# Kernel optimization log

Hardware: AMD Instinct MI355X
Metric: run time of the kernel (lower is better)

Reference implementation:

```python
import jax, jax.numpy as jnp
import numpy as np

NS, NV = 64, 16
IN_DIM = NS + 3 * NV + 3 * NV + NV  # 176 = 64x0e + 16x1o + 16x1e + 16x0o
W_SHAPES = {'0e': (NS + NV, NS), '1o': (NS + 2 * NV, NV), '1e': (3 * NV, NV), '0o': (2 * NV, NV)}
W_NUMEL = sum(a * b for a, b in W_SHAPES.values())  # 7936
E = 16384
S2 = float(np.sqrt(2.0))
S3 = float(np.sqrt(3.0))


def setup_inputs() -> dict:
    key = jax.random.key(0)
    k1, k2, k3 = jax.random.split(key, 3)
    in_ = jax.random.normal(k1, (E, IN_DIM), dtype=jnp.float32)
    sh = jax.random.normal(k2, (E, 4), dtype=jnp.float32)
    weight = jax.random.normal(k3, (E, W_NUMEL), dtype=jnp.float32)
    return {"in_": in_, "sh": sh, "weight": weight}


def reference(in_, sh, weight):
    lead = in_.shape[:-1]
    # split input irreps (order: 0e, 1o, 1e, 0o)
    x0e = in_[..., :NS]                                       # [..., NS]
    x1o = in_[..., NS:NS + 3 * NV].reshape(lead + (NV, 3))    # [..., NV, 3]
    x1e = in_[..., NS + 3 * NV:NS + 6 * NV].reshape(lead + (NV, 3))
    x0o = in_[..., NS + 6 * NV:]                              # [..., NV]
    sh0 = sh[..., 0]            # [...]
    sh1 = sh[..., 1:]           # [..., 3]
    sh1b = sh1[..., None, :]    # [..., 1, 3]

    # tensor-product paths
    out0e = jnp.concatenate([
        x0e * sh0[..., None],                      # 0e x 0e -> 0e
        jnp.sum(x1o * sh1b, axis=-1) / S3,         # 1o . 1o -> 0e
    ], axis=-1)                                    # [..., NS+NV]
    out1o = jnp.concatenate([
        x0e[..., :, None] * sh1b,                  # 0e x 1o -> 1o
        x1o * sh0[..., None, None],                # 1o x 0e -> 1o
        jnp.cross(x1e, sh1b) / S2,                 # 1e x 1o -> 1o
    ], axis=-2)                                    # [..., NS+2NV, 3]
    out1e = jnp.concatenate([
        jnp.cross(x1o, sh1b) / S2,                 # 1o x 1o -> 1e
        x1e * sh0[..., None, None],                # 1e x 0e -> 1e
        x0o[..., :, None] * sh1b,                  # 0o x 1o -> 1e
    ], axis=-2)                                    # [..., 3NV, 3]
    out0o = jnp.concatenate([
        jnp.sum(x1e * sh1b, axis=-1) / S3,         # 1e . 1o -> 0o
        x0o * sh0[..., None],                      # 0o x 0e -> 0o
    ], axis=-1)                                    # [..., 2NV]

    # per-edge weights, split and path-normalized by 1/sqrt(fan_in)
    wd, off = {}, 0
    for k, (a, b) in W_SHAPES.items():
        wd[k] = weight[..., off:off + a * b].reshape(lead + (a, b)) / float(np.sqrt(a))
        off += a * b

    y0e = jnp.einsum('...i,...io->...o', out0e, wd['0e'])                     # [..., NS]
    y1o = jnp.einsum('...ic,...io->...oc', out1o, wd['1o']).reshape(lead + (3 * NV,))
    y1e = jnp.einsum('...ic,...io->...oc', out1e, wd['1e']).reshape(lead + (3 * NV,))
    y0o = jnp.einsum('...i,...io->...o', out0o, wd['0o'])                     # [..., NV]

    return jnp.concatenate([y0e, y1o, y1e, y0o], axis=-1)  # [..., 176]
```

## Files before the change

### kernel.cpp

```cpp
#include <hip/hip_runtime.h>
#include <math.h>

#define NS 64
#define NV 16
#define IN_DIM 176
#define W_NUMEL 7936
#define OUT_DIM 176

#define OFF_0E 0
#define OFF_1O 5120
#define OFF_1E 6656
#define OFF_0O 7424

__global__ __launch_bounds__(256)
void ftp_kernel(const float* __restrict__ in_,
                const float* __restrict__ sh,
                const float* __restrict__ weight,
                float* __restrict__ out)
{
    __shared__ float s_in[IN_DIM];
    __shared__ float s_sh4[4];
    __shared__ float s_o0e[80];
    __shared__ float s_o1o[96 * 3];
    __shared__ float s_o1e[48 * 3];
    __shared__ float s_o0o[32];

    const int row = blockIdx.x;
    const int t = threadIdx.x;
    const float* __restrict__ inr  = in_    + (size_t)row * IN_DIM;
    const float* __restrict__ wr   = weight + (size_t)row * W_NUMEL;
    float* __restrict__       outr = out    + (size_t)row * OUT_DIM;

    if (t < IN_DIM) s_in[t] = inr[t];
    if (t >= 176 && t < 180) s_sh4[t - 176] = sh[(size_t)row * 4 + (t - 176)];
    __syncthreads();

    const float sh0 = s_sh4[0];
    const float sh1_0 = s_sh4[1], sh1_1 = s_sh4[2], sh1_2 = s_sh4[3];
    const float sh1[3] = {sh1_0, sh1_1, sh1_2};
    const float inv_s3 = 0.5773502691896258f;
    const float inv_s2 = 0.7071067811865476f;

    for (int j = t; j < 544; j += 256) {
        if (j < 80) {
            int i = j;
            float val;
            if (i < 64) {
                val = s_in[i] * sh0;
            } else {
                int v = i - 64;
                val = (s_in[64 + v*3 + 0] * sh1_0 +
                       s_in[64 + v*3 + 1] * sh1_1 +
                       s_in[64 + v*3 + 2] * sh1_2) * inv_s3;
            }
            s_o0e[i] = val;
        } else if (j < 368) {
            int jj = j - 80;
            int i = jj / 3, c = jj % 3;
            float val;
            if (i < 64) {
                val = s_in[i] * sh1[c];
            } else if (i < 80) {
                int v = i - 64;
                val = s_in[64 + v*3 + c] * sh0;
            } else {
                int v = i - 80;
                int c1 = (c + 1) % 3, c2 = (c + 2) % 3;
                val = (s_in[112 + v*3 + c1] * sh1[c2] -
                       s_in[112 + v*3 + c2] * sh1[c1]) * inv_s2;
            }
            s_o1o[jj] = val;
        } else if (j < 512) {
            int jj = j - 368;
            int i = jj / 3, c = jj % 3;
            float val;
            if (i < 16) {
                int v = i;
                int c1 = (c + 1) % 3, c2 = (c + 2) % 3;
                val = (s_in[64 + v*3 + c1] * sh1[c2] -
                       s_in[64 + v*3 + c2] * sh1[c1]) * inv_s2;
            } else if (i < 32) {
                int v = i - 16;
                val = s_in[112 + v*3 + c] * sh0;
            } else {
                int v = i - 32;
                val = s_in[160 + v] * sh1[c];
            }
            s_o1e[jj] = val;
        } else {
            int i = j - 512;
            float val;
            if (i < 16) {
                val = (s_in[112 + i*3 + 0] * sh1_0 +
                       s_in[112 + i*3 + 1] * sh1_1 +
                       s_in[112 + i*3 + 2] * sh1_2) * inv_s3;
            } else {
                val = s_in[160 + (i - 16)] * sh0;
            }
            s_o0o[i] = val;
        }
    }
    __syncthreads();

    const int wave = t >> 6;
    const int l = t & 63;

    if (wave < 2) {
        const int o4 = (wave << 3) + (l & 7);
        const int g  = l >> 3;
        float ax = 0.f, ay = 0.f, az = 0.f, aw = 0.f;
        #pragma unroll
        for (int k = 0; k < 10; ++k) {
            const int i = g + (k << 3);
            const float4 w4 = *reinterpret_cast<const float4*>(wr + OFF_0E + i*64 + 4*o4);
            const float s = s_o0e[i];
            ax += w4.x * s; ay += w4.y * s; az += w4.z * s; aw += w4.w * s;
        }
        #pragma unroll
        for (int m = 8; m <= 32; m <<= 1) {
            ax += __shfl_xor(ax, m);
            ay += __shfl_xor(ay, m);
            az += __shfl_xor(az, m);
            aw += __shfl_xor(aw, m);
        }
        if (g == 0) {
            const float n = 0.11180339887498949f;
            float4 r; r.x = ax*n; r.y = ay*n; r.z = az*n; r.w = aw*n;
            *reinterpret_cast<float4*>(outr + 4*o4) = r;
        }
    } else if (wave == 2) {
        const int o4 = l & 3;
        const int g  = l >> 2;
        float a0x=0,a0y=0,a0z=0,a0w=0;
        float a1x=0,a1y=0,a1z=0,a1w=0;
        float a2x=0,a2y=0,a2z=0,a2w=0;
        #pragma unroll
        for (int k = 0; k < 6; ++k) {
            const int i = g + (k << 4);
            const float4 w4 = *reinterpret_cast<const float4*>(wr + OFF_1O + i*16 + 4*o4);
            const float s0 = s_o1o[i*3 + 0];
            const float s1 = s_o1o[i*3 + 1];
            const float s2 = s_o1o[i*3 + 2];
            a0x += w4.x*s0; a0y += w4.y*s0; a0z += w4.z*s0; a0w += w4.w*s0;
            a1x += w4.x*s1; a1y += w4.y*s1; a1z += w4.z*s1; a1w += w4.w*s1;
            a2x += w4.x*s2; a2y += w4.y*s2; a2z += w4.z*s2; a2w += w4.w*s2;
        }
        #pragma unroll
        for (int m = 4; m <= 32; m <<= 1) {
            a0x += __shfl_xor(a0x, m); a0y += __shfl_xor(a0y, m);
            a0z += __shfl_xor(a0z, m); a0w += __shfl_xor(a0w, m);
            a1x += __shfl_xor(a1x, m); a1y += __shfl_xor(a1y, m);
            a1z += __shfl_xor(a1z, m); a1w += __shfl_xor(a1w, m);
            a2x += __shfl_xor(a2x, m); a2y += __shfl_xor(a2y, m);
            a2z += __shfl_xor(a2z, m); a2w += __shfl_xor(a2w, m);
        }
        if (g == 0) {
            const float n = 0.10206207261596575f;
            const int ob = 4*o4;
            outr[64 + (ob+0)*3 + 0] = a0x*n; outr[64 + (ob+0)*3 + 1] = a1x*n; outr[64 + (ob+0)*3 + 2] = a2x*n;
            outr[64 + (ob+1)*3 + 0] = a0y*n; outr[64 + (ob+1)*3 + 1] = a1y*n; outr[64 + (ob+1)*3 + 2] = a2y*n;
            outr[64 + (ob+2)*3 + 0] = a0z*n; outr[64 + (ob+2)*3 + 1] = a1z*n; outr[64 + (ob+2)*3 + 2] = a2z*n;
            outr[64 + (ob+3)*3 + 0] = a0w*n; outr[64 + (ob+3)*3 + 1] = a1w*n; outr[64 + (ob+3)*3 + 2] = a2w*n;
        }
    } else {
        {
            const int o4 = l & 3;
            const int g  = l >> 2;
            float a0x=0,a0y=0,a0z=0,a0w=0;
            float a1x=0,a1y=0,a1z=0,a1w=0;
            float a2x=0,a2y=0,a2z=0,a2w=0;
            #pragma unroll
            for (int k = 0; k < 3; ++k) {
                const int i = g + (k << 4);
                const float4 w4 = *reinterpret_cast<const float4*>(wr + OFF_1E + i*16 + 4*o4);
                const float s0 = s_o1e[i*3 + 0];
                const float s1 = s_o1e[i*3 + 1];
                const float s2 = s_o1e[i*3 + 2];
                a0x += w4.x*s0; a0y += w4.y*s0; a0z += w4.z*s0; a0w += w4.w*s0;
                a1x += w4.x*s1; a1y += w4.y*s1; a1z += w4.z*s1; a1w += w4.w*s1;
                a2x += w4.x*s2; a2y += w4.y*s2; a2z += w4.z*s2; a2w += w4.w*s2;
            }
            #pragma unroll
            for (int m = 4; m <= 32; m <<= 1) {
                a0x += __shfl_xor(a0x, m); a0y += __shfl_xor(a0y, m);
                a0z += __shfl_xor(a0z, m); a0w += __shfl_xor(a0w, m);
                a1x += __shfl_xor(a1x, m); a1y += __shfl_xor(a1y, m);
                a1z += __shfl_xor(a1z, m); a1w += __shfl_xor(a1w, m);
                a2x += __shfl_xor(a2x, m); a2y += __shfl_xor(a2y, m);
                a2z += __shfl_xor(a2z, m); a2w += __shfl_xor(a2w, m);
            }
            if (g == 0) {
                const float n = 0.14433756729740643f;
                const int ob = 4*o4;
                outr[112 + (ob+0)*3 + 0] = a0x*n; outr[112 + (ob+0)*3 + 1] = a1x*n; outr[112 + (ob+0)*3 + 2] = a2x*n;
                outr[112 + (ob+1)*3 + 0] = a0y*n; outr[112 + (ob+1)*3 + 1] = a1y*n; outr[112 + (ob+1)*3 + 2] = a2y*n;
                outr[112 + (ob+2)*3 + 0] = a0z*n; outr[112 + (ob+2)*3 + 1] = a1z*n; outr[112 + (ob+2)*3 + 2] = a2z*n;
                outr[112 + (ob+3)*3 + 0] = a0w*n; outr[112 + (ob+3)*3 + 1] = a1w*n; outr[112 + (ob+3)*3 + 2] = a2w*n;
            }
        }
        {
            const int o4 = l & 3;
            const int g  = l >> 2;
            float ax = 0.f, ay = 0.f, az = 0.f, aw = 0.f;
            #pragma unroll
            for (int k = 0; k < 2; ++k) {
                const int i = g + (k << 4);
                const float4 w4 = *reinterpret_cast<const float4*>(wr + OFF_0O + i*16 + 4*o4);
                const float s = s_o0o[i];
                ax += w4.x * s; ay += w4.y * s; az += w4.z * s; aw += w4.w * s;
            }
            #pragma unroll
            for (int m = 4; m <= 32; m <<= 1) {
                ax += __shfl_xor(ax, m);
                ay += __shfl_xor(ay, m);
                az += __shfl_xor(az, m);
                aw += __shfl_xor(aw, m);
            }
            if (g == 0) {
                const float n = 0.17677669529663687f;
                float4 r; r.x = ax*n; r.y = ay*n; r.z = az*n; r.w = aw*n;
                *reinterpret_cast<float4*>(outr + 160 + 4*o4) = r;
            }
        }
    }
}

extern "C" void kernel_launch(void* const* d_in, const int* in_sizes, int n_in,
                              void* d_out, int out_size, void* d_ws, size_t ws_size,
                              hipStream_t stream) {
    const float* in_    = (const float*)d_in[0];
    const float* sh     = (const float*)d_in[1];
    const float* weight = (const float*)d_in[2];
    float* out = (float*)d_out;
    const int E = in_sizes[0] / IN_DIM;

    ftp_kernel<<<E, 256, 0, stream>>>(in_, sh, weight, out);
}
```

Measured before the change: 98.85 us.

## Drop block barriers; per-wave input staging with weight loads issued first

Each wave now loads the row's input itself into a private LDS slice and syncs with a wave barrier instead of two block-wide __syncthreads. All weight float4 loads are issued before staging, so global latency overlaps the input fetch. Each wave computes its own tensor-product coefficients in registers instead of going through a shared intermediate buffer. The 1e and 0o reductions are merged into one shuffle loop. The cost is redundant input loads per wave and higher register pressure.

```diff
diff --git a/kernel.cpp b/kernel.cpp
--- a/kernel.cpp
+++ b/kernel.cpp
@@ -1,8 +1,5 @@
 #include <hip/hip_runtime.h>
-#include <math.h>
-
-#define NS 64
-#define NV 16
+
 #define IN_DIM 176
 #define W_NUMEL 7936
 #define OUT_DIM 176
@@ -18,110 +15,65 @@
                 const float* __restrict__ weight,
                 float* __restrict__ out)
 {
-    __shared__ float s_in[IN_DIM];
-    __shared__ float s_sh4[4];
-    __shared__ float s_o0e[80];
-    __shared__ float s_o1o[96 * 3];
-    __shared__ float s_o1e[48 * 3];
-    __shared__ float s_o0o[32];
+    __shared__ float s_in[4 * 192];
 
     const int row = blockIdx.x;
     const int t = threadIdx.x;
-    const float* __restrict__ inr  = in_    + (size_t)row * IN_DIM;
-    const float* __restrict__ wr   = weight + (size_t)row * W_NUMEL;
-    float* __restrict__       outr = out    + (size_t)row * OUT_DIM;
-
-    if (t < IN_DIM) s_in[t] = inr[t];
-    if (t >= 176 && t < 180) s_sh4[t - 176] = sh[(size_t)row * 4 + (t - 176)];
-    __syncthreads();
-
-    const float sh0 = s_sh4[0];
-    const float sh1_0 = s_sh4[1], sh1_1 = s_sh4[2], sh1_2 = s_sh4[3];
-    const float sh1[3] = {sh1_0, sh1_1, sh1_2};
+    const int wave = t >> 6;
+    const int l = t & 63;
+
+    const float* __restrict__ inr = in_    + (size_t)row * IN_DIM;
+    const float* __restrict__ wr  = weight + (size_t)row * W_NUMEL;
+    float* __restrict__       outr= out    + (size_t)row * OUT_DIM;
+    const float* __restrict__ shr = sh     + (size_t)row * 4;
+
+    float* s_my = &s_in[wave * 192];
+
+    const float a0 = inr[l];
+    const float a1 = inr[64 + l];
+    const float a2 = (l < 48) ? inr[128 + l] : 0.0f;
+
+    const float sh0   = shr[0];
+    const float sh1_0 = shr[1], sh1_1 = shr[2], sh1_2 = shr[3];
+
     const float inv_s3 = 0.5773502691896258f;
     const float inv_s2 = 0.7071067811865476f;
 
-    for (int j = t; j < 544; j += 256) {
-        if (j < 80) {
-            int i = j;
-            float val;
-            if (i < 64) {
-                val = s_in[i] * sh0;
-            } else {
-                int v = i - 64;
-                val = (s_in[64 + v*3 + 0] * sh1_0 +
-                       s_in[64 + v*3 + 1] * sh1_1 +
-                       s_in[64 + v*3 + 2] * sh1_2) * inv_s3;
-            }
-            s_o0e[i] = val;
-        } else if (j < 368) {
-            int jj = j - 80;
-            int i = jj / 3, c = jj % 3;
-            float val;
-            if (i < 64) {
-                val = s_in[i] * sh1[c];
-            } else if (i < 80) {
-                int v = i - 64;
-                val = s_in[64 + v*3 + c] * sh0;
-            } else {
-                int v = i - 80;
-                int c1 = (c + 1) % 3, c2 = (c + 2) % 3;
-                val = (s_in[112 + v*3 + c1] * sh1[c2] -
-                       s_in[112 + v*3 + c2] * sh1[c1]) * inv_s2;
-            }
-            s_o1o[jj] = val;
-        } else if (j < 512) {
-            int jj = j - 368;
-            int i = jj / 3, c = jj % 3;
-            float val;
-            if (i < 16) {
-                int v = i;
-                int c1 = (c + 1) % 3, c2 = (c + 2) % 3;
-                val = (s_in[64 + v*3 + c1] * sh1[c2] -
-                       s_in[64 + v*3 + c2] * sh1[c1]) * inv_s2;
-            } else if (i < 32) {
-                int v = i - 16;
-                val = s_in[112 + v*3 + c] * sh0;
-            } else {
-                int v = i - 32;
-                val = s_in[160 + v] * sh1[c];
-            }
-            s_o1e[jj] = val;
-        } else {
-            int i = j - 512;
-            float val;
-            if (i < 16) {
-                val = (s_in[112 + i*3 + 0] * sh1_0 +
-                       s_in[112 + i*3 + 1] * sh1_1 +
-                       s_in[112 + i*3 + 2] * sh1_2) * inv_s3;
-            } else {
-                val = s_in[160 + (i - 16)] * sh0;
-            }
-            s_o0o[i] = val;
-        }
-    }
-    __syncthreads();
-
-    const int wave = t >> 6;
-    const int l = t & 63;
+#define STAGE_AND_WAIT()                                        \
+    do {                                                        \
+        s_my[l] = a0; s_my[64 + l] = a1;                        \
+        if (l < 48) s_my[128 + l] = a2;                         \
+        __builtin_amdgcn_wave_barrier();                        \
+        asm volatile("s_waitcnt lgkmcnt(0)" ::: "memory");      \
+        __builtin_amdgcn_sched_barrier(0);                      \
+    } while (0)
 
     if (wave < 2) {
         const int o4 = (wave << 3) + (l & 7);
         const int g  = l >> 3;
+        float4 w[10];
+        #pragma unroll
+        for (int k = 0; k < 10; ++k)
+            w[k] = *reinterpret_cast<const float4*>(wr + OFF_0E + (g + (k << 3)) * 64 + 4 * o4);
+
+        STAGE_AND_WAIT();
+
+        float s[10];
+        #pragma unroll
+        for (int k = 0; k < 8; ++k) s[k] = s_my[g + (k << 3)] * sh0;
+        s[8] = (s_my[64 + 3*g] * sh1_0 + s_my[65 + 3*g] * sh1_1 + s_my[66 + 3*g] * sh1_2) * inv_s3;
+        s[9] = (s_my[88 + 3*g] * sh1_0 + s_my[89 + 3*g] * sh1_1 + s_my[90 + 3*g] * sh1_2) * inv_s3;
+
         float ax = 0.f, ay = 0.f, az = 0.f, aw = 0.f;
         #pragma unroll
         for (int k = 0; k < 10; ++k) {
-            const int i = g + (k << 3);
-            const float4 w4 = *reinterpret_cast<const float4*>(wr + OFF_0E + i*64 + 4*o4);
-            const float s = s_o0e[i];
-            ax += w4.x * s; ay += w4.y * s; az += w4.z * s; aw += w4.w * s;
+            ax += w[k].x * s[k]; ay += w[k].y * s[k];
+            az += w[k].z * s[k]; aw += w[k].w * s[k];
         }
         #pragma unroll
         for (int m = 8; m <= 32; m <<= 1) {
-            ax += __shfl_xor(ax, m);
-            ay += __shfl_xor(ay, m);
-            az += __shfl_xor(az, m);
-            aw += __shfl_xor(aw, m);
+            ax += __shfl_xor(ax, m); ay += __shfl_xor(ay, m);
+            az += __shfl_xor(az, m); aw += __shfl_xor(aw, m);
         }
         if (g == 0) {
             const float n = 0.11180339887498949f;
@@ -131,19 +83,37 @@
     } else if (wave == 2) {
         const int o4 = l & 3;
         const int g  = l >> 2;
+        float4 w[6];
+        #pragma unroll
+        for (int k = 0; k < 6; ++k)
+            w[k] = *reinterpret_cast<const float4*>(wr + OFF_1O + (g + (k << 4)) * 16 + 4 * o4);
+
+        STAGE_AND_WAIT();
+
+        float s0[6], s1[6], s2[6];
+        #pragma unroll
+        for (int k = 0; k < 4; ++k) {
+            const float x = s_my[g + (k << 4)];
+            s0[k] = x * sh1_0; s1[k] = x * sh1_1; s2[k] = x * sh1_2;
+        }
+        s0[4] = s_my[64 + 3*g] * sh0;
+        s1[4] = s_my[65 + 3*g] * sh0;
+        s2[4] = s_my[66 + 3*g] * sh0;
+        {
+            const float e0 = s_my[112 + 3*g], e1 = s_my[113 + 3*g], e2 = s_my[114 + 3*g];
+            s0[5] = (e1 * sh1_2 - e2 * sh1_1) * inv_s2;
+            s1[5] = (e2 * sh1_0 - e0 * sh1_2) * inv_s2;
+            s2[5] = (e0 * sh1_1 - e1 * sh1_0) * inv_s2;
+        }
+
         float a0x=0,a0y=0,a0z=0,a0w=0;
         float a1x=0,a1y=0,a1z=0,a1w=0;
         float a2x=0,a2y=0,a2z=0,a2w=0;
         #pragma unroll
         for (int k = 0; k < 6; ++k) {
-            const int i = g + (k << 4);
-            const float4 w4 = *reinterpret_cast<const float4*>(wr + OFF_1O + i*16 + 4*o4);
-            const float s0 = s_o1o[i*3 + 0];
-            const float s1 = s_o1o[i*3 + 1];
-            const float s2 = s_o1o[i*3 + 2];
-            a0x += w4.x*s0; a0y += w4.y*s0; a0z += w4.z*s0; a0w += w4.w*s0;
-            a1x += w4.x*s1; a1y += w4.y*s1; a1z += w4.z*s1; a1w += w4.w*s1;
-            a2x += w4.x*s2; a2y += w4.y*s2; a2z += w4.z*s2; a2w += w4.w*s2;
+            a0x += w[k].x*s0[k]; a0y += w[k].y*s0[k]; a0z += w[k].z*s0[k]; a0w += w[k].w*s0[k];
+            a1x += w[k].x*s1[k]; a1y += w[k].y*s1[k]; a1z += w[k].z*s1[k]; a1w += w[k].w*s1[k];
+            a2x += w[k].x*s2[k]; a2y += w[k].y*s2[k]; a2z += w[k].z*s2[k]; a2w += w[k].w*s2[k];
         }
         #pragma unroll
         for (int m = 4; m <= 32; m <<= 1) {
@@ -163,66 +133,73 @@
             outr[64 + (ob+3)*3 + 0] = a0w*n; outr[64 + (ob+3)*3 + 1] = a1w*n; outr[64 + (ob+3)*3 + 2] = a2w*n;
         }
     } else {
+        const int o4 = l & 3;
+        const int g  = l >> 2;
+        float4 wa[3], wb[2];
+        #pragma unroll
+        for (int k = 0; k < 3; ++k)
+            wa[k] = *reinterpret_cast<const float4*>(wr + OFF_1E + (g + (k << 4)) * 16 + 4 * o4);
+        #pragma unroll
+        for (int k = 0; k < 2; ++k)
+            wb[k] = *reinterpret_cast<const float4*>(wr + OFF_0O + (g + (k << 4)) * 16 + 4 * o4);
+
+        STAGE_AND_WAIT();
+
+        float s0[3], s1[3], s2[3];
         {
-            const int o4 = l & 3;
-            const int g  = l >> 2;
-            float a0x=0,a0y=0,a0z=0,a0w=0;
-            float a1x=0,a1y=0,a1z=0,a1w=0;
-            float a2x=0,a2y=0,a2z=0,a2w=0;
-            #pragma unroll
-            for (int k = 0; k < 3; ++k) {
-                const int i = g + (k << 4);
-                const float4 w4 = *reinterpret_cast<const float4*>(wr + OFF_1E + i*16 + 4*o4);
-                const float s0 = s_o1e[i*3 + 0];
-                const float s1 = s_o1e[i*3 + 1];
-                const float s2 = s_o1e[i*3 + 2];
-                a0x += w4.x*s0; a0y += w4.y*s0; a0z += w4.z*s0; a0w += w4.w*s0;
-                a1x += w4.x*s1; a1y += w4.y*s1; a1z += w4.z*s1; a1w += w4.w*s1;
-                a2x += w4.x*s2; a2y += w4.y*s2; a2z += w4.z*s2; a2w += w4.w*s2;
-            }
-            #pragma unroll
-            for (int m = 4; m <= 32; m <<= 1) {
-                a0x += __shfl_xor(a0x, m); a0y += __shfl_xor(a0y, m);
-                a0z += __shfl_xor(a0z, m); a0w += __shfl_xor(a0w, m);
-                a1x += __shfl_xor(a1x, m); a1y += __shfl_xor(a1y, m);
-                a1z += __shfl_xor(a1z, m); a1w += __shfl_xor(a1w, m);
-                a2x += __shfl_xor(a2x, m); a2y += __shfl_xor(a2y, m);
-                a2z += __shfl_xor(a2z, m); a2w += __shfl_xor(a2w, m);
-            }
-            if (g == 0) {
-                const float n = 0.14433756729740643f;
-                const int ob = 4*o4;
-                outr[112 + (ob+0)*3 + 0] = a0x*n; outr[112 + (ob+0)*3 + 1] = a1x*n; outr[112 + (ob+0)*3 + 2] = a2x*n;
-                outr[112 + (ob+1)*3 + 0] = a0y*n; outr[112 + (ob+1)*3 + 1] = a1y*n; outr[112 + (ob+1)*3 + 2] = a2y*n;
-                outr[112 + (ob+2)*3 + 0] = a0z*n; outr[112 + (ob+2)*3 + 1] = a1z*n; outr[112 + (ob+2)*3 + 2] = a2z*n;
-                outr[112 + (ob+3)*3 + 0] = a0w*n; outr[112 + (ob+3)*3 + 1] = a1w*n; outr[112 + (ob+3)*3 + 2] = a2w*n;
-            }
-        }
+            const float o0 = s_my[64 + 3*g], o1 = s_my[65 + 3*g], o2 = s_my[66 + 3*g];
+            s0[0] = (o1 * sh1_2 - o2 * sh1_1) * inv_s2;
+            s1[0] = (o2 * sh1_0 - o0 * sh1_2) * inv_s2;
+            s2[0] = (o0 * sh1_1 - o1 * sh1_0) * inv_s2;
+        }
+        const float e0 = s_my[112 + 3*g], e1 = s_my[113 + 3*g], e2 = s_my[114 + 3*g];
+        s0[1] = e0 * sh0; s1[1] = e1 * sh0; s2[1] = e2 * sh0;
         {
-            const int o4 = l & 3;
-            const int g  = l >> 2;
-            float ax = 0.f, ay = 0.f, az = 0.f, aw = 0.f;
-            #pragma unroll
-            for (int k = 0; k < 2; ++k) {
-                const int i = g + (k << 4);
-                const float4 w4 = *reinterpret_cast<const float4*>(wr + OFF_0O + i*16 + 4*o4);
-                const float s = s_o0o[i];
-                ax += w4.x * s; ay += w4.y * s; az += w4.z * s; aw += w4.w * s;
-            }
-            #pragma unroll
-            for (int m = 4; m <= 32; m <<= 1) {
-                ax += __shfl_xor(ax, m);
-                ay += __shfl_xor(ay, m);
-                az += __shfl_xor(az, m);
-                aw += __shfl_xor(aw, m);
-            }
-            if (g == 0) {
-                const float n = 0.17677669529663687f;
-                float4 r; r.x = ax*n; r.y = ay*n; r.z = az*n; r.w = aw*n;
-                *reinterpret_cast<float4*>(outr + 160 + 4*o4) = r;
-            }
+            const float x = s_my[160 + g];
+            s0[2] = x * sh1_0; s1[2] = x * sh1_1; s2[2] = x * sh1_2;
+        }
+
+        float a0x=0,a0y=0,a0z=0,a0w=0;
+        float a1x=0,a1y=0,a1z=0,a1w=0;
+        float a2x=0,a2y=0,a2z=0,a2w=0;
+        #pragma unroll
+        for (int k = 0; k < 3; ++k) {
+            a0x += wa[k].x*s0[k]; a0y += wa[k].y*s0[k]; a0z += wa[k].z*s0[k]; a0w += wa[k].w*s0[k];
+            a1x += wa[k].x*s1[k]; a1y += wa[k].y*s1[k]; a1z += wa[k].z*s1[k]; a1w += wa[k].w*s1[k];
+            a2x += wa[k].x*s2[k]; a2y += wa[k].y*s2[k]; a2z += wa[k].z*s2[k]; a2w += wa[k].w*s2[k];
+        }
+        float sb0 = (e0 * sh1_0 + e1 * sh1_1 + e2 * sh1_2) * inv_s3;
+        float sb1 = s_my[160 + g] * sh0;
+        float bx = wb[0].x*sb0 + wb[1].x*sb1;
+        float by = wb[0].y*sb0 + wb[1].y*sb1;
+        float bz = wb[0].z*sb0 + wb[1].z*sb1;
+        float bw = wb[0].w*sb0 + wb[1].w*sb1;
+
+        #pragma unroll
+        for (int m = 4; m <= 32; m <<= 1) {
+            a0x += __shfl_xor(a0x, m); a0y += __shfl_xor(a0y, m);
+            a0z += __shfl_xor(a0z, m); a0w += __shfl_xor(a0w, m);
+            a1x += __shfl_xor(a1x, m); a1y += __shfl_xor(a1y, m);
+            a1z += __shfl_xor(a1z, m); a1w += __shfl_xor(a1w, m);
+            a2x += __shfl_xor(a2x, m); a2y += __shfl_xor(a2y, m);
+            a2z += __shfl_xor(a2z, m); a2w += __shfl_xor(a2w, m);
+            bx  += __shfl_xor(bx,  m); by  += __shfl_xor(by,  m);
+            bz  += __shfl_xor(bz,  m); bw  += __shfl_xor(bw,  m);
+        }
+        if (g == 0) {
+            const float n48 = 0.14433756729740643f;
+            const int ob = 4*o4;
+            outr[112 + (ob+0)*3 + 0] = a0x*n48; outr[112 + (ob+0)*3 + 1] = a1x*n48; outr[112 + (ob+0)*3 + 2] = a2x*n48;
+            outr[112 + (ob+1)*3 + 0] = a0y*n48; outr[112 + (ob+1)*3 + 1] = a1y*n48; outr[112 + (ob+1)*3 + 2] = a2y*n48;
+            outr[112 + (ob+2)*3 + 0] = a0z*n48; outr[112 + (ob+2)*3 + 1] = a1z*n48; outr[112 + (ob+2)*3 + 2] = a2z*n48;
+            outr[112 + (ob+3)*3 + 0] = a0w*n48; outr[112 + (ob+3)*3 + 1] = a1w*n48; outr[112 + (ob+3)*3 + 2] = a2w*n48;
+
+            const float n32 = 0.17677669529663687f;
+            float4 r; r.x = bx*n32; r.y = by*n32; r.z = bz*n32; r.w = bw*n32;
+            *reinterpret_cast<float4*>(outr + 160 + 4*o4) = r;
         }
     }
+#undef STAGE_AND_WAIT
 }
 
 extern "C" void kernel_launch(void* const* d_in, const int* in_sizes, int n_in,
```

Result: no change. 98.29 us (-0.6%).
